# Kernel optimization log

Measured on AMD Instinct MI355X. Metric: run time of the kernel, lower is better.

## Reference

```python
import jax, jax.numpy as jnp
import numpy as np


def setup_inputs() -> dict:
    key = jax.random.key(0)
    k1, k2 = jax.random.split(key)
    x = jax.random.normal(k1, (32, 128, 112, 112), dtype=jnp.float32)
    weight = jax.random.normal(k2, (256, 128, 3, 3), dtype=jnp.float32)
    return {"x": x, "weight": weight}


def reference(x, weight):
    # Equivalent to torch unfold + einsum: valid (no padding), stride-1
    # cross-correlation conv2d with no bias.
    # x: [B, Cin, H, W], weight: [Cout, Cin, kh, kw] -> [B, Cout, H-kh+1, W-kw+1]
    return jax.lax.conv_general_dilated(
        x, weight,
        window_strides=(1, 1),
        padding="VALID",
        dimension_numbers=("NCHW", "OIHW", "NCHW"),
    )
```

## Files before the change

kernel.cpp:

```cpp
#include <hip/hip_runtime.h>

typedef __attribute__((ext_vector_type(8))) short short8;
typedef __attribute__((ext_vector_type(4))) float f32x4;

#define CIN   128
#define COUT  256
#define H     112
#define W     112
#define OH    110
#define OW    110
#define KHW   9
#define TH    8
#define TW    32
#define IHH   10
#define IWW   34
#define NPIX  340
#define XB    (NPIX*128)
#define WB    16384

__device__ __forceinline__ short f2b(float f) {
  unsigned u = __builtin_bit_cast(unsigned, f);
  unsigned r = (u + 0x7FFFu + ((u >> 16) & 1u)) >> 16;
  return (short)r;
}

typedef unsigned int u32;
__device__ __forceinline__ void gload16(const void* g, void* l) {
  __builtin_amdgcn_global_load_lds(
      (const __attribute__((address_space(1))) u32*)g,
      (__attribute__((address_space(3))) u32*)l, 16, 0, 0);
}


template<bool USE_WT>
__global__ __launch_bounds__(512, 4)
void conv_main(const float* __restrict__ x, const float* __restrict__ wgt,
               const short* __restrict__ wt, float* __restrict__ out) {
  __shared__ __align__(16) char smem[XB + 2*WB];
  char* sx = smem;
  char* sw = smem + XB;

  const int tid = threadIdx.x;

  const int nb  = gridDim.x;
  const int swz = (blockIdx.x & 7) * (nb >> 3) + (blockIdx.x >> 3);
  const int b    = swz / 112;
  const int rem  = swz - b * 112;
  const int cblk = rem / 56;
  const int rem2 = rem - cblk * 56;
  const int t_w  = rem2 / 14;
  const int t_h  = rem2 - t_w * 14;
  const int h0 = t_h * TH, w0 = t_w * TW;

  const float* xb = x + (size_t)b * CIN * (H*W);

  auto stage_x = [&](int hh) {
    const float* xh = xb + (size_t)(hh * 64) * (H*W);
    for (int u = tid; u < 8 * NPIX; u += 512) {
      int G = u / NPIX, p = u - G * NPIX;
      int iy = p / IWW, ix = p - iy * IWW;
      int gy = h0 + iy, gx = w0 + ix;
      short8 v = {0,0,0,0,0,0,0,0};
      if (gy < H && gx < W) {
        const float* s = xh + (size_t)(G*8) * (H*W) + gy * W + gx;
        #pragma unroll
        for (int j = 0; j < 8; ++j) v[j] = f2b(s[j * (H*W)]);
      }
      *(short8*)(sx + p*128 + ((G ^ (p & 7)) << 4)) = v;
    }
  };

  auto stage_w = [&](int st, int buf) {
    int hh = st / 9, tap = st - hh * 9;
    if (USE_WT) {
      const short* base = wt + (size_t)tap * (COUT*CIN)
                             + (size_t)(cblk*128) * CIN + hh * 64;
      #pragma unroll
      for (int it = 0; it < 2; ++it) {
        int slot = it * 512 + tid;
        int c = slot >> 3, gsw = (slot & 7) ^ (c & 7);
        gload16(base + c * CIN + gsw * 8, sw + buf*WB + slot * 16);
      }
    } else {
      #pragma unroll
      for (int it = 0; it < 2; ++it) {
        int slot = it * 512 + tid;
        int c = slot >> 3, gsw = (slot & 7) ^ (c & 7);
        int cout = cblk*128 + c;
        short8 v;
        #pragma unroll
        for (int j = 0; j < 8; ++j) {
          int cin = hh*64 + gsw*8 + j;
          v[j] = f2b(wgt[cout*(CIN*KHW) + cin*KHW + (st - hh*9)]);
        }
        *(short8*)(sw + buf*WB + slot * 16) = v;
      }
    }
  };

  const int lane = tid & 63;
  const int wid  = tid >> 6;
  const int wm = wid >> 2;
  const int wn = wid & 3;
  const int l15 = lane & 15;
  const int kgrp = lane >> 4;

  f32x4 acc[4][4] = {};

  stage_x(0);
  stage_w(0, 0);
  __syncthreads();

  for (int st = 0; st < 18; ++st) {
    if (st + 1 < 18) stage_w(st + 1, (st + 1) & 1);

    const int tap = st % 9;
    const int kh = tap / 3, kw = tap - (tap/3)*3;
    const char* swb = sw + (st & 1) * WB;

    #pragma unroll
    for (int s = 0; s < 2; ++s) {
      const int g = s*4 + kgrp;
      const int aslot = (g ^ (l15 & 7)) << 4;
      short8 a[4];
      #pragma unroll
      for (int mi = 0; mi < 4; ++mi)
        a[mi] = *(const short8*)(swb + (wm*64 + mi*16 + l15) * 128 + aslot);
      short8 bf[4];
      #pragma unroll
      for (int ni = 0; ni < 4; ++ni) {
        int p = (2*wn + (ni >> 1) + kh) * IWW + (ni & 1)*16 + l15 + kw;
        bf[ni] = *(const short8*)(sx + p*128 + ((g ^ (p & 7)) << 4));
      }
      #pragma unroll
      for (int mi = 0; mi < 4; ++mi)
        #pragma unroll
        for (int ni = 0; ni < 4; ++ni)
          acc[mi][ni] = __builtin_amdgcn_mfma_f32_16x16x32_bf16(a[mi], bf[ni], acc[mi][ni], 0, 0, 0);
    }

    if (st == 8) {
      __syncthreads();
      stage_x(1);
      __syncthreads();
    } else {
      __syncthreads();
    }
  }

  float* ob = out + (size_t)b * COUT * (OH*OW);
  #pragma unroll
  for (int ni = 0; ni < 4; ++ni) {
    int oh = h0 + 2*wn + (ni >> 1);
    int ow = w0 + (ni & 1)*16 + l15;
    if (oh < OH && ow < OW) {
      #pragma unroll
      for (int mi = 0; mi < 4; ++mi) {
        #pragma unroll
        for (int r = 0; r < 4; ++r) {
          int cout = cblk*128 + wm*64 + mi*16 + kgrp*4 + r;
          ob[(size_t)cout*(OH*OW) + oh*OW + ow] = acc[mi][ni][r];
        }
      }
    }
  }
}

__global__ void wprep(const float* __restrict__ wgt, short* __restrict__ wt) {
  int idx = blockIdx.x * 256 + threadIdx.x;
  if (idx >= KHW*COUT*CIN) return;
  int khw  = idx / (COUT*CIN);
  int rem  = idx - khw*(COUT*CIN);
  int cout = rem >> 7, cin = rem & 127;
  wt[idx] = f2b(wgt[cout*(CIN*KHW) + cin*KHW + khw]);
}

extern "C" void kernel_launch(void* const* d_in, const int* in_sizes, int n_in,
                              void* d_out, int out_size, void* d_ws, size_t ws_size,
                              hipStream_t stream) {
  const float* x   = (const float*)d_in[0];
  const float* wgt = (const float*)d_in[1];
  float* out = (float*)d_out;
  const size_t wt_bytes = (size_t)(KHW*COUT*CIN) * sizeof(short);
  dim3 grid(3584);
  if (ws_size >= wt_bytes) {
    short* wt = (short*)d_ws;
    wprep<<<(KHW*COUT*CIN + 255)/256, 256, 0, stream>>>(wgt, wt);
    conv_main<true><<<grid, 512, 0, stream>>>(x, wgt, wt, out);
  } else {
    conv_main<false><<<grid, 512, 0, stream>>>(x, wgt, nullptr, out);
  }
}
```

Before: 344.3 us.

## Pre-transpose input to NHWC bf16 and stage tiles via direct global-to-LDS loads

New measurement: 372.9 us. +8.3%, slower.

```diff
diff --git a/kernel.cpp b/kernel.cpp
--- a/kernel.cpp
+++ b/kernel.cpp
@@ -2,6 +2,7 @@
 
 typedef __attribute__((ext_vector_type(8))) short short8;
 typedef __attribute__((ext_vector_type(4))) float f32x4;
+typedef unsigned int u32;
 
 #define CIN   128
 #define COUT  256
@@ -15,7 +16,7 @@
 #define IHH   10
 #define IWW   34
 #define NPIX  340
-#define XB    (NPIX*128)
+#define XB    (NPIX*8*16)
 #define WB    16384
 
 __device__ __forceinline__ short f2b(float f) {
@@ -24,7 +25,6 @@
   return (short)r;
 }
 
-typedef unsigned int u32;
 __device__ __forceinline__ void gload16(const void* g, void* l) {
   __builtin_amdgcn_global_load_lds(
       (const __attribute__((address_space(1))) u32*)g,
@@ -32,10 +32,11 @@
 }
 
 
-template<bool USE_WT>
+template<bool XT, bool WT>
 __global__ __launch_bounds__(512, 4)
 void conv_main(const float* __restrict__ x, const float* __restrict__ wgt,
-               const short* __restrict__ wt, float* __restrict__ out) {
+               const short* __restrict__ wt, const short* __restrict__ xt,
+               const short* __restrict__ zp, float* __restrict__ out) {
   __shared__ __align__(16) char smem[XB + 2*WB];
   char* sx = smem;
   char* sw = smem + XB;
@@ -52,27 +53,47 @@
   const int t_h  = rem2 - t_w * 14;
   const int h0 = t_h * TH, w0 = t_w * TW;
 
-  const float* xb = x + (size_t)b * CIN * (H*W);
-
   auto stage_x = [&](int hh) {
-    const float* xh = xb + (size_t)(hh * 64) * (H*W);
-    for (int u = tid; u < 8 * NPIX; u += 512) {
-      int G = u / NPIX, p = u - G * NPIX;
-      int iy = p / IWW, ix = p - iy * IWW;
-      int gy = h0 + iy, gx = w0 + ix;
-      short8 v = {0,0,0,0,0,0,0,0};
-      if (gy < H && gx < W) {
-        const float* s = xh + (size_t)(G*8) * (H*W) + gy * W + gx;
-        #pragma unroll
-        for (int j = 0; j < 8; ++j) v[j] = f2b(s[j * (H*W)]);
-      }
-      *(short8*)(sx + p*128 + ((G ^ (p & 7)) << 4)) = v;
-    }
+    if (XT) {
+      const short* xtb = xt + (size_t)b * (H*W*CIN);
+      #pragma unroll
+      for (int it = 0; it < 6; ++it) {
+        int u = it*512 + tid;
+        if (u < 8*NPIX) {
+          int G = u / NPIX, p = u - G*NPIX;
+          int iy = p / IWW, ix = p - iy * IWW;
+          int gy = h0 + iy, gx = w0 + ix;
+          const short* src = (gy < H && gx < W)
+              ? xtb + ((size_t)gy*W + gx)*CIN + hh*64 + G*8
+              : zp;
+          gload16(src, sx + u*16);
+        }
+      }
+    } else {
+      const float* xh = x + (size_t)b * CIN * (H*W) + (size_t)(hh*64) * (H*W);
+      for (int u = tid; u < 8 * NPIX; u += 512) {
+        int G = u / NPIX, p = u - G * NPIX;
+        int iy = p / IWW, ix = p - iy * IWW;
+        int gy = h0 + iy, gx = w0 + ix;
+        short8 v = {0,0,0,0,0,0,0,0};
+        if (gy < H && gx < W) {
+          const float* s = xh + (size_t)(G*8) * (H*W) + gy * W + gx;
+          #pragma unroll
+          for (int j = 0; j < 8; ++j) v[j] = f2b(s[j * (H*W)]);
+        }
+        *(short8*)(sx + p*128 + ((G ^ (p & 7)) << 4)) = v;
+      }
+    }
+  };
+
+  auto bx_addr = [&](int g, int p) -> const char* {
+    if (XT) return sx + (g*NPIX + p) * 16;
+    else    return sx + p*128 + ((g ^ (p & 7)) << 4);
   };
 
   auto stage_w = [&](int st, int buf) {
     int hh = st / 9, tap = st - hh * 9;
-    if (USE_WT) {
+    if (WT) {
       const short* base = wt + (size_t)tap * (COUT*CIN)
                              + (size_t)(cblk*128) * CIN + hh * 64;
       #pragma unroll
@@ -91,7 +112,7 @@
         #pragma unroll
         for (int j = 0; j < 8; ++j) {
           int cin = hh*64 + gsw*8 + j;
-          v[j] = f2b(wgt[cout*(CIN*KHW) + cin*KHW + (st - hh*9)]);
+          v[j] = f2b(wgt[cout*(CIN*KHW) + cin*KHW + tap]);
         }
         *(short8*)(sw + buf*WB + slot * 16) = v;
       }
@@ -130,7 +151,7 @@
       #pragma unroll
       for (int ni = 0; ni < 4; ++ni) {
         int p = (2*wn + (ni >> 1) + kh) * IWW + (ni & 1)*16 + l15 + kw;
-        bf[ni] = *(const short8*)(sx + p*128 + ((g ^ (p & 7)) << 4));
+        bf[ni] = *(const short8*)bx_addr(g, p);
       }
       #pragma unroll
       for (int mi = 0; mi < 4; ++mi)
@@ -166,13 +187,36 @@
   }
 }
 
-__global__ void wprep(const float* __restrict__ wgt, short* __restrict__ wt) {
+__global__ void wprep(const float* __restrict__ wgt, short* __restrict__ wt,
+                      short* __restrict__ zp) {
   int idx = blockIdx.x * 256 + threadIdx.x;
+  if (idx < 128) zp[idx] = 0;
   if (idx >= KHW*COUT*CIN) return;
   int khw  = idx / (COUT*CIN);
   int rem  = idx - khw*(COUT*CIN);
   int cout = rem >> 7, cin = rem & 127;
   wt[idx] = f2b(wgt[cout*(CIN*KHW) + cin*KHW + khw]);
+}
+
+__global__ __launch_bounds__(256)
+void xprep(const float* __restrict__ x, short* __restrict__ xt) {
+  __shared__ short lsh[CIN * 113];
+  const int bh = blockIdx.x;
+  const int b = bh / H, h = bh - b * H;
+  const float* src = x + ((size_t)b * CIN * H + h) * W;
+  for (int u = threadIdx.x; u < CIN * W; u += 256) {
+    int c = u / W, w = u - c * W;
+    lsh[c * 113 + w] = f2b(src[(size_t)c * (H*W) + w]);
+  }
+  __syncthreads();
+  short* dst = xt + (size_t)bh * (W * CIN);
+  for (int o = threadIdx.x; o < W * CIN / 8; o += 256) {
+    int w = o >> 4, s = o & 15;
+    short8 v;
+    #pragma unroll
+    for (int j = 0; j < 8; ++j) v[j] = lsh[(s*8 + j) * 113 + w];
+    *(short8*)(dst + o * 8) = v;
+  }
 }
 
 extern "C" void kernel_launch(void* const* d_in, const int* in_sizes, int n_in,
@@ -182,12 +226,22 @@
   const float* wgt = (const float*)d_in[1];
   float* out = (float*)d_out;
   const size_t wt_bytes = (size_t)(KHW*COUT*CIN) * sizeof(short);
+  const size_t zp_bytes = 256;
+  const size_t xt_bytes = (size_t)32 * H * W * CIN * sizeof(short);
   dim3 grid(3584);
-  if (ws_size >= wt_bytes) {
+  if (ws_size >= wt_bytes + zp_bytes + xt_bytes) {
     short* wt = (short*)d_ws;
-    wprep<<<(KHW*COUT*CIN + 255)/256, 256, 0, stream>>>(wgt, wt);
-    conv_main<true><<<grid, 512, 0, stream>>>(x, wgt, wt, out);
+    short* zp = (short*)((char*)d_ws + wt_bytes);
+    short* xt = (short*)((char*)d_ws + wt_bytes + zp_bytes);
+    wprep<<<(KHW*COUT*CIN + 255)/256, 256, 0, stream>>>(wgt, wt, zp);
+    xprep<<<32 * H, 256, 0, stream>>>(x, xt);
+    conv_main<true, true><<<grid, 512, 0, stream>>>(x, wgt, wt, xt, zp, out);
+  } else if (ws_size >= wt_bytes + zp_bytes) {
+    short* wt = (short*)d_ws;
+    short* zp = (short*)((char*)d_ws + wt_bytes);
+    wprep<<<(KHW*COUT*CIN + 255)/256, 256, 0, stream>>>(wgt, wt, zp);
+    conv_main<false, true><<<grid, 512, 0, stream>>>(x, wgt, wt, nullptr, zp, out);
   } else {
-    conv_main<false><<<grid, 512, 0, stream>>>(x, wgt, nullptr, out);
-  }
-}
+    conv_main<false, false><<<grid, 512, 0, stream>>>(x, wgt, nullptr, nullptr, nullptr, out);
+  }
+}
```
